# Kernel optimization log

Hardware: AMD Instinct MI355X
Metric: run time of the kernel (lower is better)

The kernel has to match this reference:

```python
import jax, jax.numpy as jnp
import numpy as np

B, T, I, H, K = 32, 1024, 512, 512, 2


def _causal_conv1d(x_bit, w_hik, b_h):
    # x_bit: [B, I, T]; left-pad K-1 zeros (ConstantPad1d((K-1, 0)))
    xp = jnp.pad(x_bit, ((0, 0), (0, 0), (K - 1, 0)))
    y = jax.lax.conv_general_dilated(
        xp, w_hik, window_strides=(1,), padding='VALID',
        dimension_numbers=('NCH', 'OIH', 'NCH'))  # [B, H, T]
    return y + b_h[None, :, None]


def setup_inputs() -> dict:
    key = jax.random.key(0)
    k1, k2, k3 = jax.random.split(key, 3)
    bound = 1.0 / np.sqrt(I * K)  # torch Conv1d default init scale
    return {
        'inputs': jax.random.normal(k1, (B, T, I), dtype=jnp.float32),
        'init_state': jnp.zeros((B, H), dtype=jnp.float32),
        'Wz': jax.random.uniform(k2, (H, I, K), jnp.float32, -bound, bound),
        'bz': jnp.zeros((H,), dtype=jnp.float32),
        'Wf': jax.random.uniform(k3, (H, I, K), jnp.float32, -bound, bound),
        'bf': jnp.zeros((H,), dtype=jnp.float32),
    }


def reference(inputs, init_state, Wz, bz, Wf, bf):
    # init_state is accepted but unused in the original forward (mode='f').
    x = inputs.transpose(0, 2, 1)                      # [B, I, T]
    raw_f = _causal_conv1d(x, Wf, bf).transpose(0, 2, 1)  # [B, T, H]
    raw_z = _causal_conv1d(x, Wz, bz).transpose(0, 2, 1)  # [B, T, H]

    log_f = jax.nn.log_sigmoid(raw_f)
    log_one_minus_f = jax.nn.log_sigmoid(-raw_f)
    log_z = jax.nn.log_sigmoid(raw_z)

    # recurrent_gates[t] = sum_{s>t} log_f[s]  (suffix sum of log_f over time, excluding t=0 shift)
    rg = log_f[:, 1:, :]                               # [B, T-1, H]
    cs = jnp.cumsum(rg, axis=1)
    rg = rg - cs + cs[:, -1:, :]
    rg = jnp.concatenate([rg, jnp.zeros((inputs.shape[0], 1, rg.shape[2]), dtype=rg.dtype)], axis=1)  # [B, T, H]

    log_hidden = jax.lax.cumlogsumexp(log_z + log_one_minus_f + rg, axis=1)
    hidden = jnp.exp(log_hidden - rg)
    return hidden
```

## Files before the change

kernel.cpp:

```cpp
#include <hip/hip_runtime.h>
#include <hip/hip_bf16.h>
#include <cstddef>
#include <cstdint>

#define B_  32
#define T_  1024
#define I_  512
#define H_  512
#define M_  (B_ * T_)
#define TP_ 1025

typedef __bf16 bf16x8  __attribute__((ext_vector_type(8)));
typedef float  floatx4 __attribute__((ext_vector_type(4)));

__device__ __forceinline__ unsigned short f2bf(float f) {
    uint32_t u = __float_as_uint(f);
    return (unsigned short)((u + 0x7FFFu + ((u >> 16) & 1u)) >> 16);
}
__device__ __forceinline__ float bf2f_lo(uint32_t p) { return __uint_as_float(p << 16); }
__device__ __forceinline__ float bf2f_hi(uint32_t p) { return __uint_as_float(p & 0xFFFF0000u); }
__device__ __forceinline__ float sigm(float x) {
    return __builtin_amdgcn_rcpf(1.f + __expf(-x));
}

#define GLL(src, dst) __builtin_amdgcn_global_load_lds( \
    (const __attribute__((address_space(1))) void*)(src), \
    (__attribute__((address_space(3))) void*)(dst), 16, 0, 0)

#define NB_BUILD 16400
#define NB_PACK  4096

__global__ __launch_bounds__(256) void prep(const float* __restrict__ x,
                                            const float* __restrict__ Wf,
                                            const float* __restrict__ Wz,
                                            unsigned short* __restrict__ Ab2,
                                            unsigned short* __restrict__ Wp) {
    if (blockIdx.x < NB_BUILD) {
        int g = blockIdx.x * 256 + threadIdx.x;
        int idx4 = g << 2;
        int row = idx4 >> 9;
        int col = idx4 & 511;
        int b    = (int)((unsigned)row / TP_);
        int trow = row - b * TP_;
        ushort4 o = make_ushort4(0, 0, 0, 0);
        if (trow > 0) {
            float4 v = *(const float4*)&x[((size_t)b * T_ + (trow - 1)) * I_ + col];
            o.x = f2bf(v.x); o.y = f2bf(v.y); o.z = f2bf(v.z); o.w = f2bf(v.w);
        }
        *(ushort4*)&Ab2[(size_t)idx4] = o;
    } else {
        int e = (blockIdx.x - NB_BUILD) * 256 + threadIdx.x;
        int gate = e >> 19;
        int e2   = e & 524287;
        int ksub = e2 >> 14;
        int h    = (e2 >> 5) & 511;
        int kw   = e2 & 31;
        int kk   = ksub * 32 + kw;
        int tap  = kk >> 9;
        int i    = kk & 511;
        const float* G = gate ? Wz : Wf;
        Wp[e] = f2bf(G[h * (I_ * 2) + i * 2 + tap]);
    }
}

__global__ __launch_bounds__(256, 2) void mfma_gemm(
        const unsigned short* __restrict__ Ab2,
        const unsigned short* __restrict__ Wp,
        const float* __restrict__ biasF,
        const float* __restrict__ biasZ,
        unsigned short* __restrict__ rawF,
        unsigned short* __restrict__ rawZ,
        float* __restrict__ chA, float* __restrict__ chC) {
    __shared__ unsigned short smem[24576];

    const int id  = blockIdx.x;
    const int xcd = id & 7;
    const int j   = id >> 3;
    const int mi  = xcd * 32 + (j >> 2);
    const int ni  = j & 3;
    const int m0  = mi * 128;
    const int h0  = ni * 128;

    const int tid  = threadIdx.x;
    const int lane = tid & 63;
    const int wave = tid >> 6;
    const int wm   = wave >> 1, wn = wave & 1;
    const int lm   = lane & 15, quad = lane >> 4;

    const int c0 = wave * 128 + lane;
    const int c1 = c0 + 64;
    const int r0 = c0 >> 2, q0 = (c0 & 3) ^ ((r0 >> 2) & 3);
    const int r1 = c1 >> 2, q1 = (c1 & 3) ^ ((r1 >> 2) & 3);

    const int browBase = (m0 >> 10) * TP_ + (m0 & 1023);

    const unsigned short* WpF = Wp;
    const unsigned short* WpZ = Wp + 524288;

    const unsigned short* pA0 = Ab2 + (size_t)(browBase + r0) * 512 + q0 * 8;
    const unsigned short* pA1 = Ab2 + (size_t)(browBase + r1) * 512 + q1 * 8;
    const unsigned short* pF0 = WpF + (size_t)(h0 + r0) * 32 + q0 * 8;
    const unsigned short* pF1 = WpF + (size_t)(h0 + r1) * 32 + q1 * 8;
    const unsigned short* pZ0 = WpZ + (size_t)(h0 + r0) * 32 + q0 * 8;
    const unsigned short* pZ1 = WpZ + (size_t)(h0 + r1) * 32 + q1 * 8;

    unsigned short* dA0 = smem + wave * 1024;
    unsigned short* dA1 = smem + wave * 1024 + 512;
    unsigned short* dF0 = smem + 4096 + wave * 1024;
    unsigned short* dF1 = smem + 4096 + wave * 1024 + 512;
    unsigned short* dZ0 = smem + 8192 + wave * 1024;
    unsigned short* dZ1 = smem + 8192 + wave * 1024 + 512;

    int offA[4], offB[4];
    #pragma unroll
    for (int r = 0; r < 4; ++r) {
        int ml = wm * 64 + r * 16 + lm;
        offA[r] = (4 * ml + (quad ^ ((ml >> 2) & 3))) * 8;
    }
    #pragma unroll
    for (int c = 0; c < 4; ++c) {
        int nl = wn * 64 + c * 16 + lm;
        offB[c] = 4096 + (4 * nl + (quad ^ ((nl >> 2) & 3))) * 8;
    }

    floatx4 accF[4][4] = {};
    floatx4 accZ[4][4] = {};

    for (int kt2 = 0; kt2 < 16; ++kt2) {
        const int tap = kt2 >> 3;
        const int i0  = (kt2 & 7) * 64;
        #pragma unroll
        for (int s = 0; s < 2; ++s) {
            const int aoff = tap * 512 + i0 + s * 32;
            const size_t woff = (size_t)(kt2 * 2 + s) * 16384;
            const int ls = s * 12288;
            GLL(pA0 + aoff, dA0 + ls);
            GLL(pA1 + aoff, dA1 + ls);
            GLL(pF0 + woff, dF0 + ls);
            GLL(pF1 + woff, dF1 + ls);
            GLL(pZ0 + woff, dZ0 + ls);
            GLL(pZ1 + woff, dZ1 + ls);
        }
        __syncthreads();

        #pragma unroll
        for (int s = 0; s < 2; ++s) {
            const int ls = s * 12288;
            bf16x8 af[4], bF[4], bZ[4];
            #pragma unroll
            for (int r = 0; r < 4; ++r) af[r] = *(const bf16x8*)(smem + ls + offA[r]);
            #pragma unroll
            for (int c = 0; c < 4; ++c) {
                bF[c] = *(const bf16x8*)(smem + ls + offB[c]);
                bZ[c] = *(const bf16x8*)(smem + ls + offB[c] + 4096);
            }
            #pragma unroll
            for (int r = 0; r < 4; ++r) {
                #pragma unroll
                for (int c = 0; c < 4; ++c) {
                    accF[r][c] = __builtin_amdgcn_mfma_f32_16x16x32_bf16(
                                    af[r], bF[c], accF[r][c], 0, 0, 0);
                    accZ[r][c] = __builtin_amdgcn_mfma_f32_16x16x32_bf16(
                                    af[r], bZ[c], accZ[r][c], 0, 0, 0);
                }
            }
        }
        __syncthreads();
    }

    float bfv[4], bzv[4];
    #pragma unroll
    for (int c = 0; c < 4; ++c) {
        int hc = h0 + wn * 64 + c * 16 + lm;
        bfv[c] = biasF[hc];
        bzv[c] = biasZ[hc];
    }

    float2* seg = (float2*)smem;
    const int col0 = h0 + wn * 64 + lm;
    #pragma unroll
    for (int r = 0; r < 4; ++r) {
        #pragma unroll
        for (int c = 0; c < 4; ++c) {
            float A = 1.f, C = 0.f;
            #pragma unroll
            for (int v = 0; v < 4; ++v) {
                const size_t row = (size_t)(m0 + wm * 64 + r * 16 + quad * 4 + v);
                float rf = accF[r][c][v];
                float rz = accZ[r][c][v];
                rawF[row * H_ + col0 + c * 16] = f2bf(rf);
                rawZ[row * H_ + col0 + c * 16] = f2bf(rz);
                float f = sigm(rf + bfv[c]);
                float z = sigm(rz + bzv[c]);
                A *= f;
                C = fmaf(f, C - z, z);
            }
            seg[(((wave * 4 + r) * 4 + quad) * 4 + c) * 16 + lm] = make_float2(A, C);
        }
    }
    __syncthreads();

    const int b   = m0 >> 10;
    const int ckb = (m0 & 1023) >> 5;
    #pragma unroll
    for (int pp = 0; pp < 2; ++pp) {
        int p  = tid + pp * 256;
        int ck = p >> 7, hh = p & 127;
        int wv = ((ck >> 1) << 1) + (hh >> 6);
        int cc = (hh >> 4) & 3, lmm = hh & 15;
        float A = 1.f, C = 0.f;
        #pragma unroll
        for (int s = 0; s < 8; ++s) {
            int r = ((ck & 1) << 1) + (s >> 2), q = s & 3;
            float2 sc = seg[(((wv * 4 + r) * 4 + q) * 4 + cc) * 16 + lmm];
            C = fmaf(sc.x, C, sc.y);
            A *= sc.x;
        }
        size_t o = (size_t)(ckb + ck) * 16384 + (b << 9) + h0 + hh;
        chA[o] = A;
        chC[o] = C;
    }
}

__global__ __launch_bounds__(256) void scan_pass2(
        const float* __restrict__ chA, const float* __restrict__ chC,
        float* __restrict__ Hin) {
    int bh = blockIdx.x * 256 + threadIdx.x;
    float H = 0.f;
    #pragma unroll
    for (int ck = 0; ck < 32; ++ck) {
        Hin[ck * 16384 + bh] = H;
        H = fmaf(chA[ck * 16384 + bh], H, chC[ck * 16384 + bh]);
    }
}

__global__ __launch_bounds__(256) void scan_pass3(
        const unsigned short* __restrict__ rawF, const unsigned short* __restrict__ rawZ,
        const float* __restrict__ biasF, const float* __restrict__ biasZ,
        const float* __restrict__ Hin, float* __restrict__ out) {
    int g  = blockIdx.x * 256 + threadIdx.x;
    int hp = g & 255;
    int b  = (g >> 8) & 31;
    int ck = g >> 13;
    int h0 = hp * 2;
    const float bf0 = biasF[h0], bf1 = biasF[h0 + 1];
    const float bz0 = biasZ[h0], bz1 = biasZ[h0 + 1];
    size_t base = ((size_t)(b * T_ + ck * 32)) * H_ + h0;
    float2 hin = *(const float2*)&Hin[(size_t)ck * 16384 + (b << 9) + h0];
    float hs0 = hin.x, hs1 = hin.y;
    #pragma unroll 8
    for (int s = 0; s < 32; ++s) {
        uint32_t pf = *(const uint32_t*)&rawF[base + (size_t)s * H_];
        uint32_t pz = *(const uint32_t*)&rawZ[base + (size_t)s * H_];
        float f0 = sigm(bf2f_lo(pf) + bf0);
        float f1 = sigm(bf2f_hi(pf) + bf1);
        float z0 = sigm(bf2f_lo(pz) + bz0);
        float z1 = sigm(bf2f_hi(pz) + bz1);
        hs0 = fmaf(f0, hs0 - z0, z0);
        hs1 = fmaf(f1, hs1 - z1, z1);
        *(float2*)&out[base + (size_t)s * H_] = make_float2(hs0, hs1);
    }
}

extern "C" void kernel_launch(void* const* d_in, const int* in_sizes, int n_in,
                              void* d_out, int out_size, void* d_ws, size_t ws_size,
                              hipStream_t stream) {
    const float* x  = (const float*)d_in[0];
    const float* Wz = (const float*)d_in[2];
    const float* bz = (const float*)d_in[3];
    const float* Wf = (const float*)d_in[4];
    const float* bf = (const float*)d_in[5];
    float* out = (float*)d_out;

    char* ws = (char*)d_ws;
    unsigned short* Ab2  = (unsigned short*)(ws);
    unsigned short* rawF = (unsigned short*)(ws + (size_t)34  * 1024 * 1024);
    unsigned short* rawZ = (unsigned short*)(ws + (size_t)66  * 1024 * 1024);
    unsigned short* Wp   = (unsigned short*)(ws + (size_t)98  * 1024 * 1024);
    float*          chA  = (float*)(ws + (size_t)100 * 1024 * 1024);
    float*          chC  = (float*)(ws + (size_t)102 * 1024 * 1024);
    float*          Hin  = (float*)(ws + (size_t)104 * 1024 * 1024);

    prep<<<NB_BUILD + NB_PACK, 256, 0, stream>>>(x, Wf, Wz, Ab2, Wp);

    mfma_gemm<<<1024, 256, 0, stream>>>(Ab2, Wp, bf, bz, rawF, rawZ, chA, chC);

    scan_pass2<<<16384 / 256, 256, 0, stream>>>(chA, chC, Hin);
    scan_pass3<<<262144 / 256, 256, 0, stream>>>(rawF, rawZ, bf, bz, Hin, out);
}
```

Before: 224.6 us.

## Fuse scan into GEMM with decoupled chained lookback across time tiles

Merges the GEMM with the two scan passes. Each block takes a dynamic virtual ID, computes per-tile gate products and carries, waits on a flag from the previous time tile in its chain, publishes its outgoing hidden state, and then writes the final output straight from registers. This removes the bf16 rawF/rawZ round trip through memory and two extra kernel launches. The cost is a serial dependency chain of length 8 through global flags, plus a memset. The prep kernel is also changed to write 8 elements per thread.

```diff
diff --git a/kernel.cpp b/kernel.cpp
--- a/kernel.cpp
+++ b/kernel.cpp
@@ -12,13 +12,12 @@
 
 typedef __bf16 bf16x8  __attribute__((ext_vector_type(8)));
 typedef float  floatx4 __attribute__((ext_vector_type(4)));
+typedef unsigned short ushort8v __attribute__((ext_vector_type(8)));
 
 __device__ __forceinline__ unsigned short f2bf(float f) {
     uint32_t u = __float_as_uint(f);
     return (unsigned short)((u + 0x7FFFu + ((u >> 16) & 1u)) >> 16);
 }
-__device__ __forceinline__ float bf2f_lo(uint32_t p) { return __uint_as_float(p << 16); }
-__device__ __forceinline__ float bf2f_hi(uint32_t p) { return __uint_as_float(p & 0xFFFF0000u); }
 __device__ __forceinline__ float sigm(float x) {
     return __builtin_amdgcn_rcpf(1.f + __expf(-x));
 }
@@ -27,8 +26,8 @@
     (const __attribute__((address_space(1))) void*)(src), \
     (__attribute__((address_space(3))) void*)(dst), 16, 0, 0)
 
-#define NB_BUILD 16400
-#define NB_PACK  4096
+#define NB_BUILD 8200
+#define NB_PACK  512
 
 __global__ __launch_bounds__(256) void prep(const float* __restrict__ x,
                                             const float* __restrict__ Wf,
@@ -37,51 +36,64 @@
                                             unsigned short* __restrict__ Wp) {
     if (blockIdx.x < NB_BUILD) {
         int g = blockIdx.x * 256 + threadIdx.x;
-        int idx4 = g << 2;
-        int row = idx4 >> 9;
-        int col = idx4 & 511;
+        int idx8 = g << 3;
+        int row = idx8 >> 9;
+        int col = idx8 & 511;
         int b    = (int)((unsigned)row / TP_);
         int trow = row - b * TP_;
-        ushort4 o = make_ushort4(0, 0, 0, 0);
+        ushort8v o = {0, 0, 0, 0, 0, 0, 0, 0};
         if (trow > 0) {
-            float4 v = *(const float4*)&x[((size_t)b * T_ + (trow - 1)) * I_ + col];
-            o.x = f2bf(v.x); o.y = f2bf(v.y); o.z = f2bf(v.z); o.w = f2bf(v.w);
-        }
-        *(ushort4*)&Ab2[(size_t)idx4] = o;
+            const float* src = &x[((size_t)b * T_ + (trow - 1)) * I_ + col];
+            float4 v0 = *(const float4*)src;
+            float4 v1 = *(const float4*)(src + 4);
+            o[0] = f2bf(v0.x); o[1] = f2bf(v0.y); o[2] = f2bf(v0.z); o[3] = f2bf(v0.w);
+            o[4] = f2bf(v1.x); o[5] = f2bf(v1.y); o[6] = f2bf(v1.z); o[7] = f2bf(v1.w);
+        }
+        *(ushort8v*)&Ab2[(size_t)idx8] = o;
     } else {
-        int e = (blockIdx.x - NB_BUILD) * 256 + threadIdx.x;
-        int gate = e >> 19;
-        int e2   = e & 524287;
+        int g = (blockIdx.x - NB_BUILD) * 256 + threadIdx.x;
+        int e8   = g << 3;
+        int gate = e8 >> 19;
+        int e2   = e8 & 524287;
         int ksub = e2 >> 14;
         int h    = (e2 >> 5) & 511;
-        int kw   = e2 & 31;
-        int kk   = ksub * 32 + kw;
-        int tap  = kk >> 9;
-        int i    = kk & 511;
+        int kw0  = e2 & 31;
         const float* G = gate ? Wz : Wf;
-        Wp[e] = f2bf(G[h * (I_ * 2) + i * 2 + tap]);
-    }
-}
-
-__global__ __launch_bounds__(256, 2) void mfma_gemm(
+        ushort8v o;
+        #pragma unroll
+        for (int j = 0; j < 8; ++j) {
+            int kk  = ksub * 32 + kw0 + j;
+            int tap = kk >> 9;
+            int i   = kk & 511;
+            o[j] = f2bf(G[h * (I_ * 2) + i * 2 + tap]);
+        }
+        *(ushort8v*)&Wp[(size_t)e8] = o;
+    }
+}
+
+__global__ __launch_bounds__(256, 2) void mfma_gemm_scan(
         const unsigned short* __restrict__ Ab2,
         const unsigned short* __restrict__ Wp,
         const float* __restrict__ biasF,
         const float* __restrict__ biasZ,
-        unsigned short* __restrict__ rawF,
-        unsigned short* __restrict__ rawZ,
-        float* __restrict__ chA, float* __restrict__ chC) {
+        float* __restrict__ out,
+        float* __restrict__ Hpub,
+        uint32_t* __restrict__ flags,
+        uint32_t* __restrict__ counter) {
     __shared__ unsigned short smem[24576];
-
-    const int id  = blockIdx.x;
-    const int xcd = id & 7;
-    const int j   = id >> 3;
-    const int mi  = xcd * 32 + (j >> 2);
-    const int ni  = j & 3;
-    const int m0  = mi * 128;
-    const int h0  = ni * 128;
-
-    const int tid  = threadIdx.x;
+    __shared__ uint32_t vid_s;
+
+    const int tid = threadIdx.x;
+    if (tid == 0) vid_s = atomicAdd(counter, 1u);
+    __syncthreads();
+    const int vid   = (int)vid_s;
+    const int pos   = vid >> 7;
+    const int chain = vid & 127;
+    const int b     = chain & 31;
+    const int ni    = chain >> 5;
+    const int h0    = ni * 128;
+    const int browBase = b * TP_ + pos * 128;
+
     const int lane = tid & 63;
     const int wave = tid >> 6;
     const int wm   = wave >> 1, wn = wave & 1;
@@ -91,8 +103,6 @@
     const int c1 = c0 + 64;
     const int r0 = c0 >> 2, q0 = (c0 & 3) ^ ((r0 >> 2) & 3);
     const int r1 = c1 >> 2, q1 = (c1 & 3) ^ ((r1 >> 2) & 3);
-
-    const int browBase = (m0 >> 10) * TP_ + (m0 & 1023);
 
     const unsigned short* WpF = Wp;
     const unsigned short* WpZ = Wp + 524288;
@@ -176,89 +186,91 @@
         bzv[c] = biasZ[hc];
     }
 
-    float2* seg = (float2*)smem;
-    const int col0 = h0 + wn * 64 + lm;
+    float2* seg  = (float2*)smem;
+    float*  hinL = (float*)&smem[16384];
+
     #pragma unroll
     for (int r = 0; r < 4; ++r) {
+        const int sid = wm * 16 + r * 4 + quad;
         #pragma unroll
         for (int c = 0; c < 4; ++c) {
             float A = 1.f, C = 0.f;
             #pragma unroll
             for (int v = 0; v < 4; ++v) {
-                const size_t row = (size_t)(m0 + wm * 64 + r * 16 + quad * 4 + v);
-                float rf = accF[r][c][v];
-                float rz = accZ[r][c][v];
-                rawF[row * H_ + col0 + c * 16] = f2bf(rf);
-                rawZ[row * H_ + col0 + c * 16] = f2bf(rz);
-                float f = sigm(rf + bfv[c]);
-                float z = sigm(rz + bzv[c]);
+                float f = sigm(accF[r][c][v] + bfv[c]);
+                float z = sigm(accZ[r][c][v] + bzv[c]);
+                accF[r][c][v] = f;
+                accZ[r][c][v] = z;
                 A *= f;
                 C = fmaf(f, C - z, z);
             }
-            seg[(((wave * 4 + r) * 4 + quad) * 4 + c) * 16 + lm] = make_float2(A, C);
-        }
-    }
-    __syncthreads();
-
-    const int b   = m0 >> 10;
-    const int ckb = (m0 & 1023) >> 5;
-    #pragma unroll
-    for (int pp = 0; pp < 2; ++pp) {
-        int p  = tid + pp * 256;
-        int ck = p >> 7, hh = p & 127;
-        int wv = ((ck >> 1) << 1) + (hh >> 6);
-        int cc = (hh >> 4) & 3, lmm = hh & 15;
-        float A = 1.f, C = 0.f;
-        #pragma unroll
-        for (int s = 0; s < 8; ++s) {
-            int r = ((ck & 1) << 1) + (s >> 2), q = s & 3;
-            float2 sc = seg[(((wv * 4 + r) * 4 + q) * 4 + cc) * 16 + lmm];
-            C = fmaf(sc.x, C, sc.y);
-            A *= sc.x;
-        }
-        size_t o = (size_t)(ckb + ck) * 16384 + (b << 9) + h0 + hh;
-        chA[o] = A;
-        chC[o] = C;
-    }
-}
-
-__global__ __launch_bounds__(256) void scan_pass2(
-        const float* __restrict__ chA, const float* __restrict__ chC,
-        float* __restrict__ Hin) {
-    int bh = blockIdx.x * 256 + threadIdx.x;
-    float H = 0.f;
-    #pragma unroll
-    for (int ck = 0; ck < 32; ++ck) {
-        Hin[ck * 16384 + bh] = H;
-        H = fmaf(chA[ck * 16384 + bh], H, chC[ck * 16384 + bh]);
-    }
-}
-
-__global__ __launch_bounds__(256) void scan_pass3(
-        const unsigned short* __restrict__ rawF, const unsigned short* __restrict__ rawZ,
-        const float* __restrict__ biasF, const float* __restrict__ biasZ,
-        const float* __restrict__ Hin, float* __restrict__ out) {
-    int g  = blockIdx.x * 256 + threadIdx.x;
-    int hp = g & 255;
-    int b  = (g >> 8) & 31;
-    int ck = g >> 13;
-    int h0 = hp * 2;
-    const float bf0 = biasF[h0], bf1 = biasF[h0 + 1];
-    const float bz0 = biasZ[h0], bz1 = biasZ[h0 + 1];
-    size_t base = ((size_t)(b * T_ + ck * 32)) * H_ + h0;
-    float2 hin = *(const float2*)&Hin[(size_t)ck * 16384 + (b << 9) + h0];
-    float hs0 = hin.x, hs1 = hin.y;
-    #pragma unroll 8
-    for (int s = 0; s < 32; ++s) {
-        uint32_t pf = *(const uint32_t*)&rawF[base + (size_t)s * H_];
-        uint32_t pz = *(const uint32_t*)&rawZ[base + (size_t)s * H_];
-        float f0 = sigm(bf2f_lo(pf) + bf0);
-        float f1 = sigm(bf2f_hi(pf) + bf1);
-        float z0 = sigm(bf2f_lo(pz) + bz0);
-        float z1 = sigm(bf2f_hi(pz) + bz1);
-        hs0 = fmaf(f0, hs0 - z0, z0);
-        hs1 = fmaf(f1, hs1 - z1, z1);
-        *(float2*)&out[base + (size_t)s * H_] = make_float2(hs0, hs1);
+            seg[sid * 128 + wn * 64 + c * 16 + lm] = make_float2(A, C);
+        }
+    }
+    __syncthreads();
+
+    float At = 1.f, Ct = 0.f;
+    if (tid < 128) {
+        #pragma unroll 8
+        for (int s = 0; s < 32; ++s) {
+            float2 sc = seg[s * 128 + tid];
+            Ct = fmaf(sc.x, Ct, sc.y);
+            At *= sc.x;
+        }
+    }
+
+    if (pos > 0) {
+        if (tid == 0) {
+            const uint32_t* fl = flags + (pos - 1) * 128 + chain;
+            while (__hip_atomic_load(fl, __ATOMIC_ACQUIRE, __HIP_MEMORY_SCOPE_AGENT) == 0u)
+                __builtin_amdgcn_s_sleep(8);
+        }
+        __syncthreads();
+    }
+
+    float Hin = 0.f;
+    if (tid < 128) {
+        if (pos > 0)
+            Hin = __hip_atomic_load(&Hpub[((size_t)(pos - 1) * 128 + chain) * 128 + tid],
+                                    __ATOMIC_RELAXED, __HIP_MEMORY_SCOPE_AGENT);
+        float Hout = fmaf(At, Hin, Ct);
+        __hip_atomic_store(&Hpub[((size_t)pos * 128 + chain) * 128 + tid], Hout,
+                           __ATOMIC_RELAXED, __HIP_MEMORY_SCOPE_AGENT);
+    }
+    __threadfence();
+    __syncthreads();
+    if (tid == 0 && pos < 7)
+        __hip_atomic_store(&flags[pos * 128 + chain], 1u,
+                           __ATOMIC_RELEASE, __HIP_MEMORY_SCOPE_AGENT);
+
+    if (tid < 128) {
+        float run = Hin;
+        #pragma unroll 8
+        for (int s = 0; s < 32; ++s) {
+            hinL[s * 128 + tid] = run;
+            float2 sc = seg[s * 128 + tid];
+            run = fmaf(sc.x, run, sc.y);
+        }
+    }
+    __syncthreads();
+
+    const int rowBase = b * T_ + pos * 128;
+    #pragma unroll
+    for (int r = 0; r < 4; ++r) {
+        const int sid = wm * 16 + r * 4 + quad;
+        #pragma unroll
+        for (int c = 0; c < 4; ++c) {
+            const int hc = h0 + wn * 64 + c * 16 + lm;
+            float hs = hinL[sid * 128 + (hc - h0)];
+            #pragma unroll
+            for (int v = 0; v < 4; ++v) {
+                float f = accF[r][c][v];
+                float z = accZ[r][c][v];
+                hs = fmaf(f, hs - z, z);
+                const size_t row = (size_t)(rowBase + wm * 64 + r * 16 + quad * 4 + v);
+                out[row * H_ + hc] = hs;
+            }
+        }
     }
 }
 
@@ -273,18 +285,15 @@
     float* out = (float*)d_out;
 
     char* ws = (char*)d_ws;
-    unsigned short* Ab2  = (unsigned short*)(ws);
-    unsigned short* rawF = (unsigned short*)(ws + (size_t)34  * 1024 * 1024);
-    unsigned short* rawZ = (unsigned short*)(ws + (size_t)66  * 1024 * 1024);
-    unsigned short* Wp   = (unsigned short*)(ws + (size_t)98  * 1024 * 1024);
-    float*          chA  = (float*)(ws + (size_t)100 * 1024 * 1024);
-    float*          chC  = (float*)(ws + (size_t)102 * 1024 * 1024);
-    float*          Hin  = (float*)(ws + (size_t)104 * 1024 * 1024);
+    unsigned short* Ab2   = (unsigned short*)(ws);
+    unsigned short* Wp    = (unsigned short*)(ws + (size_t)34 * 1024 * 1024);
+    float*          Hpub  = (float*)(ws + (size_t)36 * 1024 * 1024);
+    uint32_t*       flags = (uint32_t*)(ws + (size_t)37 * 1024 * 1024);
+    uint32_t*       cnt   = flags + 1024;
+
+    hipMemsetAsync(flags, 0, 8192, stream);
 
     prep<<<NB_BUILD + NB_PACK, 256, 0, stream>>>(x, Wf, Wz, Ab2, Wp);
 
-    mfma_gemm<<<1024, 256, 0, stream>>>(Ab2, Wp, bf, bz, rawF, rawZ, chA, chC);
-
-    scan_pass2<<<16384 / 256, 256, 0, stream>>>(chA, chC, Hin);
-    scan_pass3<<<262144 / 256, 256, 0, stream>>>(rawF, rawZ, bf, bz, Hin, out);
-}
+    mfma_gemm_scan<<<1024, 256, 0, stream>>>(Ab2, Wp, bf, bz, out, Hpub, flags, cnt);
+}
```

Result: slower. 430.0 us (+91.5%).
